# Kernel optimization log

Measured on AMD Instinct MI355X. Metric: run time of the kernel, lower is better.

Reference implementation:

```python
import jax, jax.numpy as jnp
import numpy as np

EPS_DIST = 1e-8   # matches 1.0/(dist + 1e-08) in the torch module
NEG_SLOPE = 0.2   # deep_gcns act_layer leakyrelu default
BN_EPS = 1e-5


def setup_inputs() -> dict:
    key = jax.random.key(0)
    ks = jax.random.split(key, 6)
    B, N, M = 8, 2048, 8192
    C, C_skip = 512, 256
    C_in = C + C_skip          # 768
    H1, H2 = 512, 256          # up_conv_nn = [768, 512, 256]
    pos = jax.random.normal(ks[0], (B, N, 3), dtype=jnp.float32)
    pos_skip = jax.random.normal(ks[1], (B, M, 3), dtype=jnp.float32)
    x = jax.random.normal(ks[2], (B, C, N), dtype=jnp.float32)
    x_skip = jax.random.normal(ks[3], (B, C_skip, M), dtype=jnp.float32)
    W1 = jax.random.normal(ks[4], (H1, C_in), dtype=jnp.float32) * (1.0 / np.sqrt(C_in))
    W2 = jax.random.normal(ks[5], (H2, H1), dtype=jnp.float32) * (1.0 / np.sqrt(H1))
    return {
        "pos": pos, "pos_skip": pos_skip, "x": x, "x_skip": x_skip,
        "W1": W1, "gamma1": jnp.ones((H1,), jnp.float32), "beta1": jnp.zeros((H1,), jnp.float32),
        "W2": W2, "gamma2": jnp.ones((H2,), jnp.float32), "beta2": jnp.zeros((H2,), jnp.float32),
    }


def _three_nn(query, ref):
    # query: [B, M, 3], ref: [B, N, 3] -> dist [B, M, 3], idx [B, M, 3]
    q2 = jnp.sum(query * query, axis=-1)                 # [B, M]
    r2 = jnp.sum(ref * ref, axis=-1)                     # [B, N]
    d2 = q2[:, :, None] + r2[:, None, :] - 2.0 * jnp.einsum('bmd,bnd->bmn', query, ref)
    neg_d2, idx = jax.lax.top_k(-d2, 3)                  # 3 smallest squared dists
    dist = jnp.sqrt(jnp.maximum(-neg_d2, 0.0))           # tp.three_nn returns L2 distance
    return dist, idx


def _three_interpolate(x, idx, weight):
    # x: [B, C, N], idx: [B, M, 3], weight: [B, M, 3] -> [B, C, M]
    xT = jnp.transpose(x, (0, 2, 1))                     # [B, N, C]
    gathered = jax.vmap(lambda f, i: f[i])(xT, idx)      # [B, M, 3, C]
    return jnp.einsum('bmkc,bmk->bcm', gathered, weight)


def _bn_act(h, gamma, beta):
    # training-mode BatchNorm1d over (batch, points) + LeakyReLU
    mean = jnp.mean(h, axis=(0, 2), keepdims=True)
    var = jnp.mean((h - mean) ** 2, axis=(0, 2), keepdims=True)
    h = (h - mean) * jax.lax.rsqrt(var + BN_EPS)
    h = h * gamma[None, :, None] + beta[None, :, None]
    return jnp.where(h >= 0, h, NEG_SLOPE * h)


def reference(pos, pos_skip, x, x_skip, W1, gamma1, beta1, W2, gamma2, beta2):
    # 3-NN of each fine point (pos_skip) among coarse points (pos)
    dist, idx = _three_nn(pos_skip, pos)
    dist_recip = 1.0 / (dist + EPS_DIST)
    norm = jnp.sum(dist_recip, axis=2, keepdims=True)
    weight = dist_recip / norm                           # [B, M, 3]
    interpolated = _three_interpolate(x, idx, weight)    # [B, C, M]
    feats = jnp.concatenate([interpolated, x_skip], axis=1)  # [B, C+C_skip, M]
    # MLP: Conv1d(k=1, bias=False) -> BN -> LeakyReLU, twice
    h = jnp.einsum('oi,bim->bom', W1, feats)
    h = _bn_act(h, gamma1, beta1)
    h = jnp.einsum('oi,bim->bom', W2, h)
    h = _bn_act(h, gamma2, beta2)
    return h  # [B, 256, M]
```

## Files before the change

### kernel.cpp

```cpp
#include <hip/hip_runtime.h>
#include <stdint.h>

#define B_    8
#define N_    2048
#define M_    8192
#define C_    512
#define CSK   256
#define CIN   768
#define H1C   512
#define H2C   256
#define NCOL  65536
typedef unsigned short u16;
typedef __attribute__((ext_vector_type(8))) short  s16x8;
typedef __attribute__((ext_vector_type(4))) float  f32x4;

__device__ inline u16 f2bf(float f) {
    unsigned u = __float_as_uint(f);
    unsigned r = (u + 0x7fffu + ((u >> 16) & 1u)) >> 16;
    return (u16)r;
}
__device__ inline float bflo(unsigned u) { return __uint_as_float(u << 16); }
__device__ inline float bfhi(unsigned u) { return __uint_as_float(u & 0xffff0000u); }

__global__ __launch_bounds__(256) void cvt_bf16_k(const float* __restrict__ in,
                                                  u16* __restrict__ out, int n4) {
    const int i = blockIdx.x * 256 + threadIdx.x;
    if (i >= n4) return;
    const float4 v = *(const float4*)(in + (size_t)i * 4);
    u16 o[4] = {f2bf(v.x), f2bf(v.y), f2bf(v.z), f2bf(v.w)};
    *(uint2*)(out + (size_t)i * 4) = *(uint2*)o;
}

__device__ inline void ins3(float d, int n,
                            float& d0, int& i0, float& d1, int& i1,
                            float& d2, int& i2) {
    const bool lt0 = d < d0, lt1 = d < d1, lt2 = d < d2;
    const float nd2 = lt1 ? d1 : (lt2 ? d : d2);
    const int   ni2 = lt1 ? i1 : (lt2 ? n : i2);
    const float nd1 = lt0 ? d0 : (lt1 ? d : d1);
    const int   ni1 = lt0 ? i0 : (lt1 ? n : i1);
    const float nd0 = lt0 ? d : d0;
    const int   ni0 = lt0 ? n : i0;
    d0 = nd0; d1 = nd1; d2 = nd2; i0 = ni0; i1 = ni1; i2 = ni2;
}

__global__ __launch_bounds__(256) void knn_kernel(const float* __restrict__ pos,
                                                  const float* __restrict__ pos_skip,
                                                  int* __restrict__ idx_out,
                                                  float* __restrict__ w_out) {
    __shared__ float rpx[N_], rpy[N_], rpz[N_], rr2[N_];
    const int b = blockIdx.y;
    const int tid = threadIdx.x;
    for (int t = tid; t < N_ * 3; t += 256) {
        const float v = pos[(size_t)b * N_ * 3 + t];
        const int n = t / 3, k = t - n * 3;
        if (k == 0) rpx[n] = v; else if (k == 1) rpy[n] = v; else rpz[n] = v;
    }
    __syncthreads();
    for (int n = tid; n < N_; n += 256)
        rr2[n] = rpx[n] * rpx[n] + rpy[n] * rpy[n] + rpz[n] * rpz[n];
    __syncthreads();

    const int q = tid >> 3;
    const int part = tid & 7;
    const int m = blockIdx.x * 32 + q;
    const size_t qoff = ((size_t)b * M_ + m) * 3;
    const float qx = pos_skip[qoff], qy = pos_skip[qoff + 1], qz = pos_skip[qoff + 2];
    const float q2x = -2.0f * qx, q2y = -2.0f * qy, q2z = -2.0f * qz;
    const float qq = qx * qx + qy * qy + qz * qz;

    float d0 = 1e30f, d1 = 1e30f, d2 = 1e30f;
    int i0 = 0, i1 = 0, i2 = 0;
#pragma unroll 4
    for (int i = 0; i < 64; ++i) {
        const int n = part * 4 + i * 32;
        const float4 xx = *(const float4*)&rpx[n];
        const float4 yy = *(const float4*)&rpy[n];
        const float4 zz = *(const float4*)&rpz[n];
        const float4 ww = *(const float4*)&rr2[n];
        const float s0 = fmaf(xx.x, q2x, fmaf(yy.x, q2y, fmaf(zz.x, q2z, ww.x)));
        const float s1 = fmaf(xx.y, q2x, fmaf(yy.y, q2y, fmaf(zz.y, q2z, ww.y)));
        const float s2 = fmaf(xx.z, q2x, fmaf(yy.z, q2y, fmaf(zz.z, q2z, ww.z)));
        const float s3 = fmaf(xx.w, q2x, fmaf(yy.w, q2y, fmaf(zz.w, q2z, ww.w)));
        ins3(s0, n + 0, d0, i0, d1, i1, d2, i2);
        ins3(s1, n + 1, d0, i0, d1, i1, d2, i2);
        ins3(s2, n + 2, d0, i0, d1, i1, d2, i2);
        ins3(s3, n + 3, d0, i0, d1, i1, d2, i2);
    }

#pragma unroll
    for (int xm = 1; xm <= 4; xm <<= 1) {
        const float od0 = __shfl_xor(d0, xm), od1 = __shfl_xor(d1, xm), od2 = __shfl_xor(d2, xm);
        const int   oi0 = __shfl_xor(i0, xm), oi1 = __shfl_xor(i1, xm), oi2 = __shfl_xor(i2, xm);
        ins3(od0, oi0, d0, i0, d1, i1, d2, i2);
        ins3(od1, oi1, d0, i0, d1, i1, d2, i2);
        ins3(od2, oi2, d0, i0, d1, i1, d2, i2);
    }

    if (part == 0) {
        const float dd0 = fmaxf(d0 + qq, 0.f);
        const float dd1 = fmaxf(d1 + qq, 0.f);
        const float dd2 = fmaxf(d2 + qq, 0.f);
        const float r0 = 1.0f / (sqrtf(dd0) + 1e-8f);
        const float r1 = 1.0f / (sqrtf(dd1) + 1e-8f);
        const float r2 = 1.0f / (sqrtf(dd2) + 1e-8f);
        const float inv = 1.0f / (r0 + r1 + r2);
        const size_t o = ((size_t)b * M_ + m) * 3;
        idx_out[o] = i0; idx_out[o + 1] = i1; idx_out[o + 2] = i2;
        w_out[o] = r0 * inv; w_out[o + 1] = r1 * inv; w_out[o + 2] = r2 * inv;
    }
}

__global__ __launch_bounds__(256) void transpose_x(const float* __restrict__ x,
                                                   u16* __restrict__ xT) {
    __shared__ float t[32][33];
    const int tx = threadIdx.x & 31, ty = threadIdx.x >> 5;
    const int n0 = blockIdx.x * 32, c0 = blockIdx.y * 32, b = blockIdx.z;
#pragma unroll
    for (int r = 0; r < 4; ++r) {
        const int c = c0 + ty + r * 8;
        t[ty + r * 8][tx] = x[((size_t)b * C_ + c) * N_ + n0 + tx];
    }
    __syncthreads();
#pragma unroll
    for (int r = 0; r < 4; ++r) {
        const int n = n0 + ty + r * 8;
        xT[((size_t)b * N_ + n) * C_ + c0 + tx] = f2bf(t[tx][ty + r * 8]);
    }
}

__global__ __launch_bounds__(256) void feats_skip(const float* __restrict__ xs,
                                                  u16* __restrict__ Feats) {
    __shared__ float t[32][33];
    const int tx = threadIdx.x & 31, ty = threadIdx.x >> 5;
    const int m0 = blockIdx.x * 32, c0 = blockIdx.y * 32, b = blockIdx.z;
#pragma unroll
    for (int r = 0; r < 4; ++r) {
        const int c = c0 + ty + r * 8;
        t[ty + r * 8][tx] = xs[((size_t)b * CSK + c) * M_ + m0 + tx];
    }
    __syncthreads();
#pragma unroll
    for (int r = 0; r < 4; ++r) {
        const int m = m0 + ty + r * 8;
        Feats[((size_t)b * M_ + m) * CIN + C_ + c0 + tx] = f2bf(t[tx][ty + r * 8]);
    }
}

__device__ inline unsigned interp_pk(unsigned a, unsigned b, unsigned c,
                                     float w0, float w1, float w2) {
    const float lo = w0 * bflo(a) + w1 * bflo(b) + w2 * bflo(c);
    const float hi = w0 * bfhi(a) + w1 * bfhi(b) + w2 * bfhi(c);
    return (unsigned)f2bf(lo) | ((unsigned)f2bf(hi) << 16);
}
__global__ __launch_bounds__(256) void feats_interp(const u16* __restrict__ xT,
                                                    const int* __restrict__ idx,
                                                    const float* __restrict__ w,
                                                    u16* __restrict__ Feats) {
    const int b = blockIdx.y;
    const int lane = threadIdx.x & 63, wv = threadIdx.x >> 6;
    for (int t = 0; t < 16; ++t) {
        const int m = blockIdx.x * 64 + wv * 16 + t;
        const size_t col = (size_t)b * M_ + m;
        const int i0 = idx[col * 3], i1 = idx[col * 3 + 1], i2 = idx[col * 3 + 2];
        const float w0 = w[col * 3], w1 = w[col * 3 + 1], w2 = w[col * 3 + 2];
        const uint4 a = *(const uint4*)(xT + ((size_t)b * N_ + i0) * C_ + lane * 8);
        const uint4 c = *(const uint4*)(xT + ((size_t)b * N_ + i1) * C_ + lane * 8);
        const uint4 d = *(const uint4*)(xT + ((size_t)b * N_ + i2) * C_ + lane * 8);
        uint4 r;
        r.x = interp_pk(a.x, c.x, d.x, w0, w1, w2);
        r.y = interp_pk(a.y, c.y, d.y, w0, w1, w2);
        r.z = interp_pk(a.z, c.z, d.z, w0, w1, w2);
        r.w = interp_pk(a.w, c.w, d.w, w0, w1, w2);
        *(uint4*)(Feats + col * CIN + lane * 8) = r;
    }
}

__device__ inline void stage64(u16* lds, const char* gbase, int ld2,
                               int lane, int wv) {
    const int slot = (lane & 7) ^ (lane >> 3);
#pragma unroll
    for (int jj = 0; jj < 4; ++jj) {
        const int chunk = jj * 4 + wv;
        const int row = chunk * 8 + (lane >> 3);
        const char* g = gbase + (size_t)row * ld2 + slot * 16;
        __builtin_amdgcn_global_load_lds(
            (const __attribute__((address_space(1))) void*)g,
            (__attribute__((address_space(3))) void*)((char*)lds + chunk * 1024),
            16, 0, 0);
    }
}

__global__ __launch_bounds__(256) void gemm1(const u16* __restrict__ A,
                                             const u16* __restrict__ Bm,
                                             u16* __restrict__ H1,
                                             float* __restrict__ ps1,
                                             float* __restrict__ pq1) {
    __shared__ __attribute__((aligned(16))) u16 As[128 * 64];
    __shared__ __attribute__((aligned(16))) u16 Bs[128 * 64];
    __shared__ float lsum[2][128], lsq[2][128];
    const int tid = threadIdx.x;
    const int lane = tid & 63, wv = tid >> 6;
    const int wr = wv >> 1, wc = wv & 1;
    const int l15 = lane & 15, l4 = lane >> 4;
    const int v = (blockIdx.x & 7) * 256 + (blockIdx.x >> 3);
    const int rowblk = v & 3, colblk = v >> 2;
    const int rowM0 = rowblk * 128, colN0 = colblk * 128;
    f32x4 acc[4][4] = {};
    const char* Ab = (const char*)(A  + (size_t)rowM0 * CIN);
    const char* Bb = (const char*)(Bm + (size_t)colN0 * CIN);

    for (int kt = 0; kt < CIN / 64; ++kt) {
        stage64(As, Ab + kt * 128, CIN * 2, lane, wv);
        stage64(Bs, Bb + kt * 128, CIN * 2, lane, wv);
        __syncthreads();
#pragma unroll
        for (int ks = 0; ks < 2; ++ks) {
            s16x8 af[4], bfr[4];
#pragma unroll
            for (int i = 0; i < 4; ++i) {
                const int R = wr * 64 + i * 16 + l15;
                const int s = ((ks << 2) | l4) ^ (R & 7);
                af[i] = *(const s16x8*)((const char*)As + R * 128 + s * 16);
            }
#pragma unroll
            for (int j = 0; j < 4; ++j) {
                const int R = wc * 64 + j * 16 + l15;
                const int s = ((ks << 2) | l4) ^ (R & 7);
                bfr[j] = *(const s16x8*)((const char*)Bs + R * 128 + s * 16);
            }
#pragma unroll
            for (int i = 0; i < 4; ++i)
#pragma unroll
                for (int j = 0; j < 4; ++j)
                    acc[i][j] = __builtin_amdgcn_mfma_f32_16x16x32_bf16(bfr[j], af[i], acc[i][j], 0, 0, 0);
        }
        __syncthreads();
    }

#pragma unroll
    for (int i = 0; i < 4; ++i) {
        const int o = rowM0 + wr * 64 + i * 16 + l15;
#pragma unroll
        for (int j = 0; j < 4; ++j) {
            const int colb = colN0 + wc * 64 + j * 16 + l4 * 4;
#pragma unroll
            for (int r = 0; r < 4; ++r)
                H1[(size_t)(colb + r) * H1C + o] = f2bf(acc[i][j][r]);
        }
    }

#pragma unroll
    for (int i = 0; i < 4; ++i) {
        float s = 0.f, q = 0.f;
#pragma unroll
        for (int j = 0; j < 4; ++j)
#pragma unroll
            for (int r = 0; r < 4; ++r) {
                const float vv = acc[i][j][r];
                s += vv; q += vv * vv;
            }
        s += __shfl_xor(s, 16); q += __shfl_xor(q, 16);
        s += __shfl_xor(s, 32); q += __shfl_xor(q, 32);
        if ((lane & 48) == 0) {
            lsum[wc][wr * 64 + i * 16 + l15] = s;
            lsq [wc][wr * 64 + i * 16 + l15] = q;
        }
    }
    __syncthreads();
    if (tid < 128) {
        const float S = lsum[0][tid] + lsum[1][tid];
        const float Q = lsq[0][tid] + lsq[1][tid];
        ps1[(size_t)(rowM0 + tid) * 512 + colblk] = S;
        pq1[(size_t)(rowM0 + tid) * 512 + colblk] = Q;
    }
}

__global__ __launch_bounds__(256) void bn1_final(const float* __restrict__ ps,
                                                 const float* __restrict__ pq,
                                                 const float* __restrict__ gamma,
                                                 const float* __restrict__ beta,
                                                 float* __restrict__ sc,
                                                 float* __restrict__ sh) {
    const int o = blockIdx.x;
    const int t = threadIdx.x;
    float S = ps[(size_t)o * 512 + t] + ps[(size_t)o * 512 + 256 + t];
    float Q = pq[(size_t)o * 512 + t] + pq[(size_t)o * 512 + 256 + t];
    __shared__ float rs[256], rq[256];
    rs[t] = S; rq[t] = Q;
    __syncthreads();
    for (int st = 128; st > 0; st >>= 1) {
        if (t < st) { rs[t] += rs[t + st]; rq[t] += rq[t + st]; }
        __syncthreads();
    }
    if (t == 0) {
        const float mean = rs[0] * (1.0f / NCOL);
        const float var  = fmaxf(rq[0] * (1.0f / NCOL) - mean * mean, 0.f);
        const float is   = rsqrtf(var + 1e-5f);
        const float s    = gamma[o] * is;
        sc[o] = s;
        sh[o] = beta[o] - mean * s;
    }
}

__device__ inline void stage2A(u16* dst, const u16* W2b, int k0,
                               int lane, int wv) {
#pragma unroll
    for (int h = 0; h < 2; ++h) {
        const int p_loc = h * 128 + wv * 16 + (lane >> 2);
        const u16* g = W2b + (size_t)p_loc * H1C + k0 + (lane & 3) * 8;
        __builtin_amdgcn_global_load_lds(
            (const __attribute__((address_space(1))) void*)g,
            (__attribute__((address_space(3))) void*)((char*)dst + (h * 512 + wv * 64) * 16),
            16, 0, 0);
    }
}

__global__ __launch_bounds__(512, 2) void gemm2(const u16* __restrict__ W2b,
                                                const u16* __restrict__ H1,
                                                const float* __restrict__ sc1,
                                                const float* __restrict__ sh1,
                                                float* __restrict__ out,
                                                float* __restrict__ ps2,
                                                float* __restrict__ pq2) {
    __shared__ __attribute__((aligned(16))) u16 As[2][256 * 32];
    __shared__ __attribute__((aligned(16))) u16 Bs[2][256 * 32];
    __shared__ float lsum[4][256], lsq[4][256];
    __shared__ float scs[512], shs[512];
    const int tid = threadIdx.x;
    const int lane = tid & 63, wv = tid >> 6;
    const int pgrp = wv & 1, cgrp = wv >> 1;
    const int l15 = lane & 15, l4 = lane >> 4;
    const int col0 = blockIdx.x * 256;
    const u16* Hb = H1 + (size_t)col0 * H1C;
    const int kb = (lane & 3) * 8;
    const int prow0 = wv * 16 + (lane >> 2);
    f32x4 acc[4][8] = {};

    scs[tid] = sc1[tid];
    shs[tid] = sh1[tid];

    stage2A(As[0], W2b, 0, lane, wv);
    uint4 nb0 = *(const uint4*)(Hb + (size_t)prow0 * H1C + kb);
    uint4 nb1 = *(const uint4*)(Hb + (size_t)(prow0 + 128) * H1C + kb);
    __syncthreads();

    auto xformB = [&](int buf, uint4 b0, uint4 b1, int k0) {
        const f32x4 s0v = *(const f32x4*)&scs[k0 + kb];
        const f32x4 s1v = *(const f32x4*)&scs[k0 + kb + 4];
        const f32x4 h0v = *(const f32x4*)&shs[k0 + kb];
        const f32x4 h1v = *(const f32x4*)&shs[k0 + kb + 4];
        const float sv[8] = {s0v[0], s0v[1], s0v[2], s0v[3], s1v[0], s1v[1], s1v[2], s1v[3]};
        const float hv[8] = {h0v[0], h0v[1], h0v[2], h0v[3], h1v[0], h1v[1], h1v[2], h1v[3]};
        uint4 bw[2] = {b0, b1};
#pragma unroll
        for (int h = 0; h < 2; ++h) {
            unsigned uu[4] = {bw[h].x, bw[h].y, bw[h].z, bw[h].w};
            unsigned rr[4];
#pragma unroll
            for (int e = 0; e < 4; ++e) {
                float f0 = fmaf(bflo(uu[e]), sv[e * 2], hv[e * 2]);
                float f1 = fmaf(bfhi(uu[e]), sv[e * 2 + 1], hv[e * 2 + 1]);
                f0 = f0 >= 0.f ? f0 : 0.2f * f0;
                f1 = f1 >= 0.f ? f1 : 0.2f * f1;
                rr[e] = (unsigned)f2bf(f0) | ((unsigned)f2bf(f1) << 16);
            }
            *(uint4*)&Bs[buf][(size_t)(h * 512 + wv * 64 + lane) * 8] = make_uint4(rr[0], rr[1], rr[2], rr[3]);
        }
    };

    xformB(0, nb0, nb1, 0);
    __syncthreads();

    int cur = 0;
    for (int step = 0; step < 16; ++step) {
        if (step < 15) {
            const int k0 = (step + 1) * 32;
            stage2A(As[cur ^ 1], W2b, k0, lane, wv);
            nb0 = *(const uint4*)(Hb + (size_t)prow0 * H1C + k0 + kb);
            nb1 = *(const uint4*)(Hb + (size_t)(prow0 + 128) * H1C + k0 + kb);
        }
        const u16* Ac = As[cur];
        const u16* Bc = Bs[cur];
        s16x8 af[8], bfr[4];
#pragma unroll
        for (int pf = 0; pf < 8; ++pf)
            af[pf] = *(const s16x8*)&Ac[(pgrp * 128 + pf * 16 + l15) * 32 + l4 * 8];
#pragma unroll
        for (int cf = 0; cf < 4; ++cf)
            bfr[cf] = *(const s16x8*)&Bc[(cgrp * 64 + cf * 16 + l15) * 32 + l4 * 8];
#pragma unroll
        for (int cf = 0; cf < 4; ++cf)
#pragma unroll
            for (int pf = 0; pf < 8; ++pf)
                acc[cf][pf] = __builtin_amdgcn_mfma_f32_16x16x32_bf16(bfr[cf], af[pf], acc[cf][pf], 0, 0, 0);
        if (step < 15) {
            xformB(cur ^ 1, nb0, nb1, (step + 1) * 32);
        }
        __syncthreads();
        cur ^= 1;
    }

    const int bidx = col0 >> 13;
    const int mb   = col0 & (M_ - 1);
#pragma unroll
    for (int cf = 0; cf < 4; ++cf) {
#pragma unroll
        for (int pf = 0; pf < 8; ++pf) {
            const int p  = pgrp * 128 + pf * 16 + l15;
            const int mm = mb + cgrp * 64 + cf * 16 + l4 * 4;
            *(f32x4*)(out + (size_t)bidx * (H2C * M_) + (size_t)p * M_ + mm) = acc[cf][pf];
        }
    }

#pragma unroll
    for (int pf = 0; pf < 8; ++pf) {
        float s = 0.f, q = 0.f;
#pragma unroll
        for (int cf = 0; cf < 4; ++cf)
#pragma unroll
            for (int r = 0; r < 4; ++r) {
                const float vv = acc[cf][pf][r];
                s += vv; q += vv * vv;
            }
        s += __shfl_xor(s, 16); q += __shfl_xor(q, 16);
        s += __shfl_xor(s, 32); q += __shfl_xor(q, 32);
        if ((lane & 48) == 0) {
            lsum[cgrp][pgrp * 128 + pf * 16 + l15] = s;
            lsq [cgrp][pgrp * 128 + pf * 16 + l15] = q;
        }
    }
    __syncthreads();
    if (tid < 256) {
        const float S = lsum[0][tid] + lsum[1][tid] + lsum[2][tid] + lsum[3][tid];
        const float Q = lsq[0][tid] + lsq[1][tid] + lsq[2][tid] + lsq[3][tid];
        ps2[(size_t)tid * 256 + blockIdx.x] = S;
        pq2[(size_t)tid * 256 + blockIdx.x] = Q;
    }
}

__global__ __launch_bounds__(256) void bn2_final(const float* __restrict__ ps,
                                                 const float* __restrict__ pq,
                                                 const float* __restrict__ gamma,
                                                 const float* __restrict__ beta,
                                                 float* __restrict__ sc,
                                                 float* __restrict__ sh) {
    const int p = blockIdx.x;
    const int t = threadIdx.x;
    float S = ps[(size_t)p * 256 + t];
    float Q = pq[(size_t)p * 256 + t];
    __shared__ float rs[256], rq[256];
    rs[t] = S; rq[t] = Q;
    __syncthreads();
    for (int st = 128; st > 0; st >>= 1) {
        if (t < st) { rs[t] += rs[t + st]; rq[t] += rq[t + st]; }
        __syncthreads();
    }
    if (t == 0) {
        const float mean = rs[0] * (1.0f / NCOL);
        const float var  = fmaxf(rq[0] * (1.0f / NCOL) - mean * mean, 0.f);
        const float is   = rsqrtf(var + 1e-5f);
        const float s    = gamma[p] * is;
        sc[p] = s;
        sh[p] = beta[p] - mean * s;
    }
}

__global__ __launch_bounds__(256) void bn_apply2(float* __restrict__ out,
                                                 const float* __restrict__ sc,
                                                 const float* __restrict__ sh) {
    const size_t i = (size_t)blockIdx.x * 256 + threadIdx.x;
    const int p = (int)((i >> 13) & (H2C - 1));
    float v = out[i];
    v = fmaf(v, sc[p], sh[p]);
    out[i] = v >= 0.f ? v : 0.2f * v;
}

extern "C" void kernel_launch(void* const* d_in, const int* in_sizes, int n_in,
                              void* d_out, int out_size, void* d_ws, size_t ws_size,
                              hipStream_t stream) {
    const float* pos      = (const float*)d_in[0];
    const float* pos_skip = (const float*)d_in[1];
    const float* x        = (const float*)d_in[2];
    const float* x_skip   = (const float*)d_in[3];
    const float* W1       = (const float*)d_in[4];
    const float* gamma1   = (const float*)d_in[5];
    const float* beta1    = (const float*)d_in[6];
    const float* W2       = (const float*)d_in[7];
    const float* gamma2   = (const float*)d_in[8];
    const float* beta2    = (const float*)d_in[9];
    float* out = (float*)d_out;

    char* ws = (char*)d_ws;
    size_t off = 0;
    auto alloc = [&](size_t bytes) {
        void* p = ws + off;
        off = (off + bytes + 255) & ~(size_t)255;
        return p;
    };
    int*   idx   = (int*)  alloc((size_t)NCOL * 3 * sizeof(int));
    float* w     = (float*)alloc((size_t)NCOL * 3 * sizeof(float));
    u16*   xT    = (u16*)  alloc((size_t)B_ * N_ * C_ * sizeof(u16));
    u16*   W1b   = (u16*)  alloc((size_t)H1C * CIN * sizeof(u16));
    u16*   W2b   = (u16*)  alloc((size_t)H2C * H1C * sizeof(u16));
    u16*   Feats = (u16*)  alloc((size_t)NCOL * CIN * sizeof(u16));
    u16*   H1    = (u16*)  alloc((size_t)NCOL * H1C * sizeof(u16));
    float* ps1   = (float*)alloc((size_t)H1C * 512 * sizeof(float));
    float* pq1   = (float*)alloc((size_t)H1C * 512 * sizeof(float));
    float* ps2   = (float*)alloc((size_t)H2C * 256 * sizeof(float));
    float* pq2   = (float*)alloc((size_t)H2C * 256 * sizeof(float));
    float* sc1   = (float*)alloc(H1C * sizeof(float));
    float* sh1   = (float*)alloc(H1C * sizeof(float));
    float* sc2   = (float*)alloc(H2C * sizeof(float));
    float* sh2   = (float*)alloc(H2C * sizeof(float));

    cvt_bf16_k<<<(H1C * CIN / 4 + 255) / 256, 256, 0, stream>>>(W1, W1b, H1C * CIN / 4);
    cvt_bf16_k<<<(H2C * H1C / 4 + 255) / 256, 256, 0, stream>>>(W2, W2b, H2C * H1C / 4);
    knn_kernel<<<dim3(M_ / 32, B_), 256, 0, stream>>>(pos, pos_skip, idx, w);
    transpose_x<<<dim3(N_ / 32, C_ / 32, B_), 256, 0, stream>>>(x, xT);
    feats_interp<<<dim3(M_ / 64, B_), 256, 0, stream>>>(xT, idx, w, Feats);
    feats_skip<<<dim3(M_ / 32, CSK / 32, B_), 256, 0, stream>>>(x_skip, Feats);
    gemm1<<<2048, 256, 0, stream>>>(W1b, Feats, H1, ps1, pq1);
    bn1_final<<<H1C, 256, 0, stream>>>(ps1, pq1, gamma1, beta1, sc1, sh1);
    gemm2<<<NCOL / 256, 512, 0, stream>>>(W2b, H1, sc1, sh1, out, ps2, pq2);
    bn2_final<<<H2C, 256, 0, stream>>>(ps2, pq2, gamma2, beta2, sc2, sh2);
    bn_apply2<<<(int)(((size_t)NCOL * H2C) / 256), 256, 0, stream>>>(out, sc2, sh2);
}
```

Measured before the change: 299.6 us.

## Fuse three-NN interpolation into gemm1 B-operand staging

Removes the separate feats_interp kernel and the full 768-channel Feats buffer. gemm1 now gathers three xT rows per column, blends them with the interpolation weights while staging the B tile into LDS, and reads the skip features from a compact 256-channel buffer. This saves writing and re-reading roughly 64 MB of interpolated features. In exchange, each of the 4 row blocks recomputes the interpolation, and the B staging now goes through registers with synchronous loads instead of async global_load_lds.

```diff
diff --git a/kernel.cpp b/kernel.cpp
--- a/kernel.cpp
+++ b/kernel.cpp
@@ -130,7 +130,7 @@
 }
 
 __global__ __launch_bounds__(256) void feats_skip(const float* __restrict__ xs,
-                                                  u16* __restrict__ Feats) {
+                                                  u16* __restrict__ Fsk) {
     __shared__ float t[32][33];
     const int tx = threadIdx.x & 31, ty = threadIdx.x >> 5;
     const int m0 = blockIdx.x * 32, c0 = blockIdx.y * 32, b = blockIdx.z;
@@ -143,7 +143,7 @@
 #pragma unroll
     for (int r = 0; r < 4; ++r) {
         const int m = m0 + ty + r * 8;
-        Feats[((size_t)b * M_ + m) * CIN + C_ + c0 + tx] = f2bf(t[tx][ty + r * 8]);
+        Fsk[((size_t)b * M_ + m) * CSK + c0 + tx] = f2bf(t[tx][ty + r * 8]);
     }
 }
 
@@ -152,28 +152,6 @@
     const float lo = w0 * bflo(a) + w1 * bflo(b) + w2 * bflo(c);
     const float hi = w0 * bfhi(a) + w1 * bfhi(b) + w2 * bfhi(c);
     return (unsigned)f2bf(lo) | ((unsigned)f2bf(hi) << 16);
-}
-__global__ __launch_bounds__(256) void feats_interp(const u16* __restrict__ xT,
-                                                    const int* __restrict__ idx,
-                                                    const float* __restrict__ w,
-                                                    u16* __restrict__ Feats) {
-    const int b = blockIdx.y;
-    const int lane = threadIdx.x & 63, wv = threadIdx.x >> 6;
-    for (int t = 0; t < 16; ++t) {
-        const int m = blockIdx.x * 64 + wv * 16 + t;
-        const size_t col = (size_t)b * M_ + m;
-        const int i0 = idx[col * 3], i1 = idx[col * 3 + 1], i2 = idx[col * 3 + 2];
-        const float w0 = w[col * 3], w1 = w[col * 3 + 1], w2 = w[col * 3 + 2];
-        const uint4 a = *(const uint4*)(xT + ((size_t)b * N_ + i0) * C_ + lane * 8);
-        const uint4 c = *(const uint4*)(xT + ((size_t)b * N_ + i1) * C_ + lane * 8);
-        const uint4 d = *(const uint4*)(xT + ((size_t)b * N_ + i2) * C_ + lane * 8);
-        uint4 r;
-        r.x = interp_pk(a.x, c.x, d.x, w0, w1, w2);
-        r.y = interp_pk(a.y, c.y, d.y, w0, w1, w2);
-        r.z = interp_pk(a.z, c.z, d.z, w0, w1, w2);
-        r.w = interp_pk(a.w, c.w, d.w, w0, w1, w2);
-        *(uint4*)(Feats + col * CIN + lane * 8) = r;
-    }
 }
 
 __device__ inline void stage64(u16* lds, const char* gbase, int ld2,
@@ -191,14 +169,19 @@
     }
 }
 
-__global__ __launch_bounds__(256) void gemm1(const u16* __restrict__ A,
-                                             const u16* __restrict__ Bm,
+__global__ __launch_bounds__(256) void gemm1(const u16* __restrict__ W1b,
+                                             const u16* __restrict__ xT,
+                                             const u16* __restrict__ Fsk,
+                                             const int* __restrict__ idx,
+                                             const float* __restrict__ w,
                                              u16* __restrict__ H1,
                                              float* __restrict__ ps1,
                                              float* __restrict__ pq1) {
     __shared__ __attribute__((aligned(16))) u16 As[128 * 64];
     __shared__ __attribute__((aligned(16))) u16 Bs[128 * 64];
     __shared__ float lsum[2][128], lsq[2][128];
+    __shared__ int   sIdx[128][3];
+    __shared__ float sW[128][3];
     const int tid = threadIdx.x;
     const int lane = tid & 63, wv = tid >> 6;
     const int wr = wv >> 1, wc = wv & 1;
@@ -206,13 +189,54 @@
     const int v = (blockIdx.x & 7) * 256 + (blockIdx.x >> 3);
     const int rowblk = v & 3, colblk = v >> 2;
     const int rowM0 = rowblk * 128, colN0 = colblk * 128;
+    const int b = colN0 >> 13;
     f32x4 acc[4][4] = {};
-    const char* Ab = (const char*)(A  + (size_t)rowM0 * CIN);
-    const char* Bb = (const char*)(Bm + (size_t)colN0 * CIN);
+    const char* Ab = (const char*)(W1b + (size_t)rowM0 * CIN);
+    const u16* xTb = xT + (size_t)b * N_ * C_;
+
+    for (int t = tid; t < 384; t += 256) {
+        const int rr = t / 3, kk = t - rr * 3;
+        const size_t gi = ((size_t)colN0 + rr) * 3 + kk;
+        sIdx[rr][kk] = idx[gi];
+        sW[rr][kk]   = w[gi];
+    }
+    __syncthreads();
+
+    const int prow = tid >> 3;
+    const int slot = tid & 7;
+    const int kk_off = slot * 8;
 
     for (int kt = 0; kt < CIN / 64; ++kt) {
         stage64(As, Ab + kt * 128, CIN * 2, lane, wv);
-        stage64(Bs, Bb + kt * 128, CIN * 2, lane, wv);
+        uint4 bp[4];
+        if (kt < 8) {
+            const int kk = kt * 64 + kk_off;
+#pragma unroll
+            for (int p = 0; p < 4; ++p) {
+                const int row = p * 32 + prow;
+                const uint4 a = *(const uint4*)(xTb + (size_t)sIdx[row][0] * C_ + kk);
+                const uint4 c = *(const uint4*)(xTb + (size_t)sIdx[row][1] * C_ + kk);
+                const uint4 d = *(const uint4*)(xTb + (size_t)sIdx[row][2] * C_ + kk);
+                const float w0 = sW[row][0], w1 = sW[row][1], w2 = sW[row][2];
+                bp[p].x = interp_pk(a.x, c.x, d.x, w0, w1, w2);
+                bp[p].y = interp_pk(a.y, c.y, d.y, w0, w1, w2);
+                bp[p].z = interp_pk(a.z, c.z, d.z, w0, w1, w2);
+                bp[p].w = interp_pk(a.w, c.w, d.w, w0, w1, w2);
+            }
+        } else {
+            const int kk = (kt - 8) * 64 + kk_off;
+#pragma unroll
+            for (int p = 0; p < 4; ++p) {
+                const int row = p * 32 + prow;
+                bp[p] = *(const uint4*)(Fsk + (size_t)(colN0 + row) * CSK + kk);
+            }
+        }
+#pragma unroll
+        for (int p = 0; p < 4; ++p) {
+            const int row = p * 32 + prow;
+            const int s = slot ^ (row & 7);
+            *(uint4*)((char*)Bs + row * 128 + s * 16) = bp[p];
+        }
         __syncthreads();
 #pragma unroll
         for (int ks = 0; ks < 2; ++ks) {
@@ -503,7 +527,7 @@
     u16*   xT    = (u16*)  alloc((size_t)B_ * N_ * C_ * sizeof(u16));
     u16*   W1b   = (u16*)  alloc((size_t)H1C * CIN * sizeof(u16));
     u16*   W2b   = (u16*)  alloc((size_t)H2C * H1C * sizeof(u16));
-    u16*   Feats = (u16*)  alloc((size_t)NCOL * CIN * sizeof(u16));
+    u16*   Fsk   = (u16*)  alloc((size_t)NCOL * CSK * sizeof(u16));
     u16*   H1    = (u16*)  alloc((size_t)NCOL * H1C * sizeof(u16));
     float* ps1   = (float*)alloc((size_t)H1C * 512 * sizeof(float));
     float* pq1   = (float*)alloc((size_t)H1C * 512 * sizeof(float));
@@ -518,9 +542,8 @@
     cvt_bf16_k<<<(H2C * H1C / 4 + 255) / 256, 256, 0, stream>>>(W2, W2b, H2C * H1C / 4);
     knn_kernel<<<dim3(M_ / 32, B_), 256, 0, stream>>>(pos, pos_skip, idx, w);
     transpose_x<<<dim3(N_ / 32, C_ / 32, B_), 256, 0, stream>>>(x, xT);
-    feats_interp<<<dim3(M_ / 64, B_), 256, 0, stream>>>(xT, idx, w, Feats);
-    feats_skip<<<dim3(M_ / 32, CSK / 32, B_), 256, 0, stream>>>(x_skip, Feats);
-    gemm1<<<2048, 256, 0, stream>>>(W1b, Feats, H1, ps1, pq1);
+    feats_skip<<<dim3(M_ / 32, CSK / 32, B_), 256, 0, stream>>>(x_skip, Fsk);
+    gemm1<<<2048, 256, 0, stream>>>(W1b, xT, Fsk, idx, w, H1, ps1, pq1);
     bn1_final<<<H1C, 256, 0, stream>>>(ps1, pq1, gamma1, beta1, sc1, sh1);
     gemm2<<<NCOL / 256, 512, 0, stream>>>(W2b, H1, sc1, sh1, out, ps2, pq2);
     bn2_final<<<H2C, 256, 0, stream>>>(ps2, pq2, gamma2, beta2, sc2, sh2);
```

Result: faster. 293.3 us (-2.1%).
